# Optimization experiments

Hardware: AMD Instinct MI355X
Metric: run time of the kernel (lower is better)

## Reference

```python
import jax, jax.numpy as jnp
import numpy as np

B, H, W = 16, 512, 512  # mask resolution; feature maps are 2H x 2W


def setup_inputs() -> dict:
    key = jax.random.key(0)
    k0, k1, k2, k3, k4 = jax.random.split(key, 5)
    mask = jax.random.uniform(k0, (B, 2, H, W), dtype=jnp.float32)
    xl_out = jax.random.normal(k1, (B, 3, 2 * H, 2 * W), dtype=jnp.float32)
    yl_out = jax.random.normal(k2, (B, 3, 2 * H, 2 * W), dtype=jnp.float32)
    conv_w = jax.random.normal(k3, (3, 3), dtype=jnp.float32) * 0.1  # 1x1 conv [out_c, in_c]
    conv_b = jax.random.normal(k4, (3,), dtype=jnp.float32) * 0.1
    return {"mask": mask, "xl_out": xl_out, "yl_out": yl_out,
            "conv_w": conv_w, "conv_b": conv_b}


def reference(mask, xl_out, yl_out, conv_w, conv_b):
    b, _, h, w = mask.shape
    up = jax.image.resize(mask, (b, 2, 2 * h, 2 * w), method="bilinear")  # [B,2,2H,2W]
    x_mask = up[:, 0:1]  # [B,1,2H,2W]
    y_mask = up[:, 1:2]
    fused = x_mask * xl_out + y_mask * yl_out  # [B,3,2H,2W]
    # 1x1 conv == channel mixing matmul, then ReLU.
    out = jnp.einsum("oi,bihw->bohw", conv_w, fused) + conv_b[None, :, None, None]
    out = jax.nn.relu(out)
    return (out, x_mask, y_mask)
```

## Files before the change

kernel.cpp:

```cpp
#include <hip/hip_runtime.h>

#define BATCH 16
#define HIN   512
#define WIN   512
#define HOUT  1024
#define WOUT  1024

#define OUT_ELEMS   ((size_t)BATCH * 3 * HOUT * WOUT)
#define MASK_ELEMS  ((size_t)BATCH * HOUT * WOUT)

typedef float f4 __attribute__((ext_vector_type(4)));

static __device__ __forceinline__ f4 relu4(f4 v) {
    v.x = fmaxf(v.x, 0.0f); v.y = fmaxf(v.y, 0.0f);
    v.z = fmaxf(v.z, 0.0f); v.w = fmaxf(v.w, 0.0f);
    return v;
}

__global__ __launch_bounds__(256) void fused_upsample_conv_kernel(
    const float* __restrict__ mask,
    const float* __restrict__ xl,
    const float* __restrict__ yl,
    const float* __restrict__ cw,
    const float* __restrict__ cb,
    float* __restrict__ out)
{
    const int tx   = threadIdx.x;
    const int half = tx >> 7;
    const int lane = tx & 127;
    const int r    = blockIdx.x;
    const int b    = blockIdx.y;
    const int oh   = 2 * r + half;

    int rA, rB; float wyA, wyB;
    if (half) { rA = r;                   rB = (r + 1 < HIN) ? r + 1 : HIN - 1; wyA = 0.75f; wyB = 0.25f; }
    else      { rA = (r > 0) ? r - 1 : 0; rB = r;                               wyA = 0.25f; wyB = 0.75f; }

    const int c0 = lane * 4;
    const int cL = (c0 > 0) ? c0 - 1 : 0;
    const int cR = (c0 + 4 < WIN) ? c0 + 4 : WIN - 1;

    const size_t mplane = (size_t)HIN * WIN;
    const float* pA0 = mask + ((size_t)b * 2 + 0) * mplane + (size_t)rA * WIN;
    const float* pB0 = mask + ((size_t)b * 2 + 0) * mplane + (size_t)rB * WIN;
    const float* pA1 = mask + ((size_t)b * 2 + 1) * mplane + (size_t)rA * WIN;
    const float* pB1 = mask + ((size_t)b * 2 + 1) * mplane + (size_t)rB * WIN;

    const f4    qA0 = *(const f4*)(pA0 + c0);
    const f4    qB0 = *(const f4*)(pB0 + c0);
    const float vL0 = wyA * pA0[cL] + wyB * pB0[cL];
    const float vR0 = wyA * pA0[cR] + wyB * pB0[cR];
    const f4    v0  = wyA * qA0 + wyB * qB0;

    const f4    qA1 = *(const f4*)(pA1 + c0);
    const f4    qB1 = *(const f4*)(pB1 + c0);
    const float vL1 = wyA * pA1[cL] + wyB * pB1[cL];
    const float vR1 = wyA * pA1[cR] + wyB * pB1[cR];
    const f4    v1  = wyA * qA1 + wyB * qB1;

    f4 xm0, xm1, ym0, ym1;
    xm0.x = 0.25f*vL0  + 0.75f*v0.x;  xm0.y = 0.75f*v0.x + 0.25f*v0.y;
    xm0.z = 0.25f*v0.x + 0.75f*v0.y;  xm0.w = 0.75f*v0.y + 0.25f*v0.z;
    xm1.x = 0.25f*v0.y + 0.75f*v0.z;  xm1.y = 0.75f*v0.z + 0.25f*v0.w;
    xm1.z = 0.25f*v0.z + 0.75f*v0.w;  xm1.w = 0.75f*v0.w + 0.25f*vR0;

    ym0.x = 0.25f*vL1  + 0.75f*v1.x;  ym0.y = 0.75f*v1.x + 0.25f*v1.y;
    ym0.z = 0.25f*v1.x + 0.75f*v1.y;  ym0.w = 0.75f*v1.y + 0.25f*v1.z;
    ym1.x = 0.25f*v1.y + 0.75f*v1.z;  ym1.y = 0.75f*v1.z + 0.25f*v1.w;
    ym1.z = 0.25f*v1.z + 0.75f*v1.w;  ym1.w = 0.75f*v1.w + 0.25f*vR1;

    const float w00 = cw[0], w01 = cw[1], w02 = cw[2];
    const float w10 = cw[3], w11 = cw[4], w12 = cw[5];
    const float w20 = cw[6], w21 = cw[7], w22 = cw[8];
    const float b0 = cb[0], b1 = cb[1], b2 = cb[2];

    const size_t oplane = (size_t)HOUT * WOUT;
    const size_t rowoff = (size_t)oh * WOUT + (size_t)lane * 8;

    const float* xb = xl + ((size_t)b * 3) * oplane + rowoff;
    const float* yb = yl + ((size_t)b * 3) * oplane + rowoff;

    const f4 x00 = __builtin_nontemporal_load((const f4*)(xb + 0 * oplane));
    const f4 x01 = __builtin_nontemporal_load((const f4*)(xb + 0 * oplane) + 1);
    const f4 x10 = __builtin_nontemporal_load((const f4*)(xb + 1 * oplane));
    const f4 x11 = __builtin_nontemporal_load((const f4*)(xb + 1 * oplane) + 1);
    const f4 x20 = __builtin_nontemporal_load((const f4*)(xb + 2 * oplane));
    const f4 x21 = __builtin_nontemporal_load((const f4*)(xb + 2 * oplane) + 1);
    const f4 y00 = __builtin_nontemporal_load((const f4*)(yb + 0 * oplane));
    const f4 y01 = __builtin_nontemporal_load((const f4*)(yb + 0 * oplane) + 1);
    const f4 y10 = __builtin_nontemporal_load((const f4*)(yb + 1 * oplane));
    const f4 y11 = __builtin_nontemporal_load((const f4*)(yb + 1 * oplane) + 1);
    const f4 y20 = __builtin_nontemporal_load((const f4*)(yb + 2 * oplane));
    const f4 y21 = __builtin_nontemporal_load((const f4*)(yb + 2 * oplane) + 1);

    const f4 f00 = xm0 * x00 + ym0 * y00;
    const f4 f01 = xm1 * x01 + ym1 * y01;
    const f4 f10 = xm0 * x10 + ym0 * y10;
    const f4 f11 = xm1 * x11 + ym1 * y11;
    const f4 f20 = xm0 * x20 + ym0 * y20;
    const f4 f21 = xm1 * x21 + ym1 * y21;

    const f4 o00 = relu4(w00*f00 + w01*f10 + w02*f20 + b0);
    const f4 o01 = relu4(w00*f01 + w01*f11 + w02*f21 + b0);
    const f4 o10 = relu4(w10*f00 + w11*f10 + w12*f20 + b1);
    const f4 o11 = relu4(w10*f01 + w11*f11 + w12*f21 + b1);
    const f4 o20 = relu4(w20*f00 + w21*f10 + w22*f20 + b2);
    const f4 o21 = relu4(w20*f01 + w21*f11 + w22*f21 + b2);

    float* ob = out + ((size_t)b * 3) * oplane + rowoff;
    __builtin_nontemporal_store(o00, (f4*)(ob + 0 * oplane));
    __builtin_nontemporal_store(o01, (f4*)(ob + 0 * oplane) + 1);
    __builtin_nontemporal_store(o10, (f4*)(ob + 1 * oplane));
    __builtin_nontemporal_store(o11, (f4*)(ob + 1 * oplane) + 1);
    __builtin_nontemporal_store(o20, (f4*)(ob + 2 * oplane));
    __builtin_nontemporal_store(o21, (f4*)(ob + 2 * oplane) + 1);

    float* xmp = out + OUT_ELEMS + (size_t)b * oplane + rowoff;
    float* ymp = out + OUT_ELEMS + MASK_ELEMS + (size_t)b * oplane + rowoff;
    __builtin_nontemporal_store(xm0, (f4*)xmp);
    __builtin_nontemporal_store(xm1, (f4*)xmp + 1);
    __builtin_nontemporal_store(ym0, (f4*)ymp);
    __builtin_nontemporal_store(ym1, (f4*)ymp + 1);
}

extern "C" void kernel_launch(void* const* d_in, const int* in_sizes, int n_in,
                              void* d_out, int out_size, void* d_ws, size_t ws_size,
                              hipStream_t stream) {
    const float* mask = (const float*)d_in[0];
    const float* xl   = (const float*)d_in[1];
    const float* yl   = (const float*)d_in[2];
    const float* cw   = (const float*)d_in[3];
    const float* cb   = (const float*)d_in[4];
    float* out = (float*)d_out;

    dim3 grid(HOUT / 2, BATCH);
    dim3 block(256);
    fused_upsample_conv_kernel<<<grid, block, 0, stream>>>(mask, xl, yl, cw, cb, out);
}
```

Measured before the change: 595.6 us.

## Specialize waves per plane/mask channel with LDS staging of masks and fused features

Restructures the block into 8 waves: six waves each stream one channel row of xl/yl with fully contiguous per-wave loads, while two waves compute the upsampled x/y masks for both output rows into LDS. After barriers the fused features are staged in LDS so each wave computes one output channel of the 1x1 conv and writes it. This aims for longer contiguous memory streams and less redundant mask work per thread, at the cost of two block barriers, about 40KB LDS per block, and the two mask waves doing different work from the others.

Result: faster. 580.3 us (-2.6%).

```diff
diff --git a/kernel.cpp b/kernel.cpp
--- a/kernel.cpp
+++ b/kernel.cpp
@@ -17,7 +17,7 @@
     return v;
 }
 
-__global__ __launch_bounds__(256) void fused_upsample_conv_kernel(
+__global__ __launch_bounds__(512, 4) void fused_upsample_conv_kernel(
     const float* __restrict__ mask,
     const float* __restrict__ xl,
     const float* __restrict__ yl,
@@ -25,102 +25,129 @@
     const float* __restrict__ cb,
     float* __restrict__ out)
 {
-    const int tx   = threadIdx.x;
-    const int half = tx >> 7;
-    const int lane = tx & 127;
-    const int r    = blockIdx.x;
-    const int b    = blockIdx.y;
-    const int oh   = 2 * r + half;
+    __shared__ float xm_l[2][WOUT];
+    __shared__ float ym_l[2][WOUT];
+    __shared__ float Fs[3][2][WOUT];
 
-    int rA, rB; float wyA, wyB;
-    if (half) { rA = r;                   rB = (r + 1 < HIN) ? r + 1 : HIN - 1; wyA = 0.75f; wyB = 0.25f; }
-    else      { rA = (r > 0) ? r - 1 : 0; rB = r;                               wyA = 0.25f; wyB = 0.75f; }
-
-    const int c0 = lane * 4;
-    const int cL = (c0 > 0) ? c0 - 1 : 0;
-    const int cR = (c0 + 4 < WIN) ? c0 + 4 : WIN - 1;
-
-    const size_t mplane = (size_t)HIN * WIN;
-    const float* pA0 = mask + ((size_t)b * 2 + 0) * mplane + (size_t)rA * WIN;
-    const float* pB0 = mask + ((size_t)b * 2 + 0) * mplane + (size_t)rB * WIN;
-    const float* pA1 = mask + ((size_t)b * 2 + 1) * mplane + (size_t)rA * WIN;
-    const float* pB1 = mask + ((size_t)b * 2 + 1) * mplane + (size_t)rB * WIN;
-
-    const f4    qA0 = *(const f4*)(pA0 + c0);
-    const f4    qB0 = *(const f4*)(pB0 + c0);
-    const float vL0 = wyA * pA0[cL] + wyB * pB0[cL];
-    const float vR0 = wyA * pA0[cR] + wyB * pB0[cR];
-    const f4    v0  = wyA * qA0 + wyB * qB0;
-
-    const f4    qA1 = *(const f4*)(pA1 + c0);
-    const f4    qB1 = *(const f4*)(pB1 + c0);
-    const float vL1 = wyA * pA1[cL] + wyB * pB1[cL];
-    const float vR1 = wyA * pA1[cR] + wyB * pB1[cR];
-    const f4    v1  = wyA * qA1 + wyB * qB1;
-
-    f4 xm0, xm1, ym0, ym1;
-    xm0.x = 0.25f*vL0  + 0.75f*v0.x;  xm0.y = 0.75f*v0.x + 0.25f*v0.y;
-    xm0.z = 0.25f*v0.x + 0.75f*v0.y;  xm0.w = 0.75f*v0.y + 0.25f*v0.z;
-    xm1.x = 0.25f*v0.y + 0.75f*v0.z;  xm1.y = 0.75f*v0.z + 0.25f*v0.w;
-    xm1.z = 0.25f*v0.z + 0.75f*v0.w;  xm1.w = 0.75f*v0.w + 0.25f*vR0;
-
-    ym0.x = 0.25f*vL1  + 0.75f*v1.x;  ym0.y = 0.75f*v1.x + 0.25f*v1.y;
-    ym0.z = 0.25f*v1.x + 0.75f*v1.y;  ym0.w = 0.75f*v1.y + 0.25f*v1.z;
-    ym1.x = 0.25f*v1.y + 0.75f*v1.z;  ym1.y = 0.75f*v1.z + 0.25f*v1.w;
-    ym1.z = 0.25f*v1.z + 0.75f*v1.w;  ym1.w = 0.75f*v1.w + 0.25f*vR1;
-
-    const float w00 = cw[0], w01 = cw[1], w02 = cw[2];
-    const float w10 = cw[3], w11 = cw[4], w12 = cw[5];
-    const float w20 = cw[6], w21 = cw[7], w22 = cw[8];
-    const float b0 = cb[0], b1 = cb[1], b2 = cb[2];
+    const int tx = threadIdx.x;
+    const int w  = tx >> 6;
+    const int l  = tx & 63;
+    const int r  = blockIdx.x;
+    const int b  = blockIdx.y;
 
     const size_t oplane = (size_t)HOUT * WOUT;
-    const size_t rowoff = (size_t)oh * WOUT + (size_t)lane * 8;
+    const size_t mplane = (size_t)HIN * WIN;
 
-    const float* xb = xl + ((size_t)b * 3) * oplane + rowoff;
-    const float* yb = yl + ((size_t)b * 3) * oplane + rowoff;
+    const int p  = w % 3;
+    const int hr = (w < 6) ? (w / 3) : 0;
+    const int oh = 2 * r + hr;
 
-    const f4 x00 = __builtin_nontemporal_load((const f4*)(xb + 0 * oplane));
-    const f4 x01 = __builtin_nontemporal_load((const f4*)(xb + 0 * oplane) + 1);
-    const f4 x10 = __builtin_nontemporal_load((const f4*)(xb + 1 * oplane));
-    const f4 x11 = __builtin_nontemporal_load((const f4*)(xb + 1 * oplane) + 1);
-    const f4 x20 = __builtin_nontemporal_load((const f4*)(xb + 2 * oplane));
-    const f4 x21 = __builtin_nontemporal_load((const f4*)(xb + 2 * oplane) + 1);
-    const f4 y00 = __builtin_nontemporal_load((const f4*)(yb + 0 * oplane));
-    const f4 y01 = __builtin_nontemporal_load((const f4*)(yb + 0 * oplane) + 1);
-    const f4 y10 = __builtin_nontemporal_load((const f4*)(yb + 1 * oplane));
-    const f4 y11 = __builtin_nontemporal_load((const f4*)(yb + 1 * oplane) + 1);
-    const f4 y20 = __builtin_nontemporal_load((const f4*)(yb + 2 * oplane));
-    const f4 y21 = __builtin_nontemporal_load((const f4*)(yb + 2 * oplane) + 1);
+    f4 xv0, xv1, xv2, xv3, yv0, yv1, yv2, yv3;
 
-    const f4 f00 = xm0 * x00 + ym0 * y00;
-    const f4 f01 = xm1 * x01 + ym1 * y01;
-    const f4 f10 = xm0 * x10 + ym0 * y10;
-    const f4 f11 = xm1 * x11 + ym1 * y11;
-    const f4 f20 = xm0 * x20 + ym0 * y20;
-    const f4 f21 = xm1 * x21 + ym1 * y21;
+    if (w < 6) {
+        const float* xp = xl + ((size_t)b * 3 + p) * oplane + (size_t)oh * WOUT;
+        const float* yp = yl + ((size_t)b * 3 + p) * oplane + (size_t)oh * WOUT;
+        xv0 = __builtin_nontemporal_load((const f4*)(xp +   0) + l);
+        xv1 = __builtin_nontemporal_load((const f4*)(xp + 256) + l);
+        xv2 = __builtin_nontemporal_load((const f4*)(xp + 512) + l);
+        xv3 = __builtin_nontemporal_load((const f4*)(xp + 768) + l);
+        yv0 = __builtin_nontemporal_load((const f4*)(yp +   0) + l);
+        yv1 = __builtin_nontemporal_load((const f4*)(yp + 256) + l);
+        yv2 = __builtin_nontemporal_load((const f4*)(yp + 512) + l);
+        yv3 = __builtin_nontemporal_load((const f4*)(yp + 768) + l);
+    } else {
+        const int ch = w - 6;
+        const float* mp = mask + ((size_t)b * 2 + ch) * mplane;
+        const int rm = (r > 0) ? r - 1 : 0;
+        const int rp = (r + 1 < HIN) ? r + 1 : HIN - 1;
+        const float* rowm = mp + (size_t)rm * WIN;
+        const float* row0 = mp + (size_t)r  * WIN;
+        const float* rowp = mp + (size_t)rp * WIN;
 
-    const f4 o00 = relu4(w00*f00 + w01*f10 + w02*f20 + b0);
-    const f4 o01 = relu4(w00*f01 + w01*f11 + w02*f21 + b0);
-    const f4 o10 = relu4(w10*f00 + w11*f10 + w12*f20 + b1);
-    const f4 o11 = relu4(w10*f01 + w11*f11 + w12*f21 + b1);
-    const f4 o20 = relu4(w20*f00 + w21*f10 + w22*f20 + b2);
-    const f4 o21 = relu4(w20*f01 + w21*f11 + w22*f21 + b2);
+        const int c0 = l * 8;
+        const int cL = (c0 > 0) ? c0 - 1 : 0;
+        const int cR = (c0 + 8 < WIN) ? c0 + 8 : WIN - 1;
 
-    float* ob = out + ((size_t)b * 3) * oplane + rowoff;
-    __builtin_nontemporal_store(o00, (f4*)(ob + 0 * oplane));
-    __builtin_nontemporal_store(o01, (f4*)(ob + 0 * oplane) + 1);
-    __builtin_nontemporal_store(o10, (f4*)(ob + 1 * oplane));
-    __builtin_nontemporal_store(o11, (f4*)(ob + 1 * oplane) + 1);
-    __builtin_nontemporal_store(o20, (f4*)(ob + 2 * oplane));
-    __builtin_nontemporal_store(o21, (f4*)(ob + 2 * oplane) + 1);
+        const f4 ma0 = *(const f4*)(rowm + c0), ma1 = *(const f4*)(rowm + c0 + 4);
+        const f4 za0 = *(const f4*)(row0 + c0), za1 = *(const f4*)(row0 + c0 + 4);
+        const f4 pa0 = *(const f4*)(rowp + c0), pa1 = *(const f4*)(rowp + c0 + 4);
+        const float mL = rowm[cL], mR = rowm[cR];
+        const float zL = row0[cL], zR = row0[cR];
+        const float pL = rowp[cL], pR = rowp[cR];
 
-    float* xmp = out + OUT_ELEMS + (size_t)b * oplane + rowoff;
-    float* ymp = out + OUT_ELEMS + MASK_ELEMS + (size_t)b * oplane + rowoff;
-    __builtin_nontemporal_store(xm0, (f4*)xmp);
-    __builtin_nontemporal_store(xm1, (f4*)xmp + 1);
-    __builtin_nontemporal_store(ym0, (f4*)ymp);
-    __builtin_nontemporal_store(ym1, (f4*)ymp + 1);
+        float* base = ch ? &ym_l[0][0] : &xm_l[0][0];
+
+        #pragma unroll
+        for (int rr = 0; rr < 2; ++rr) {
+            f4 va, vb; float vL, vR;
+            if (rr == 0) {
+                va = 0.25f * ma0 + 0.75f * za0;  vb = 0.25f * ma1 + 0.75f * za1;
+                vL = 0.25f * mL  + 0.75f * zL;   vR = 0.25f * mR  + 0.75f * zR;
+            } else {
+                va = 0.75f * za0 + 0.25f * pa0;  vb = 0.75f * za1 + 0.25f * pa1;
+                vL = 0.75f * zL  + 0.25f * pL;   vR = 0.75f * zR  + 0.25f * pR;
+            }
+            f4 o0, o1, o2, o3;
+            o0.x = 0.25f*vL   + 0.75f*va.x;  o0.y = 0.75f*va.x + 0.25f*va.y;
+            o0.z = 0.25f*va.x + 0.75f*va.y;  o0.w = 0.75f*va.y + 0.25f*va.z;
+            o1.x = 0.25f*va.y + 0.75f*va.z;  o1.y = 0.75f*va.z + 0.25f*va.w;
+            o1.z = 0.25f*va.z + 0.75f*va.w;  o1.w = 0.75f*va.w + 0.25f*vb.x;
+            o2.x = 0.25f*va.w + 0.75f*vb.x;  o2.y = 0.75f*vb.x + 0.25f*vb.y;
+            o2.z = 0.25f*vb.x + 0.75f*vb.y;  o2.w = 0.75f*vb.y + 0.25f*vb.z;
+            o3.x = 0.25f*vb.y + 0.75f*vb.z;  o3.y = 0.75f*vb.z + 0.25f*vb.w;
+            o3.z = 0.25f*vb.z + 0.75f*vb.w;  o3.w = 0.75f*vb.w + 0.25f*vR;
+            float* d = base + rr * WOUT + l * 16;
+            *(f4*)(d +  0) = o0;  *(f4*)(d +  4) = o1;
+            *(f4*)(d +  8) = o2;  *(f4*)(d + 12) = o3;
+        }
+    }
+
+    __syncthreads();
+
+    if (w < 6) {
+        const float* mx = &xm_l[hr][0];
+        const float* my = &ym_l[hr][0];
+        float* fd = &Fs[p][hr][0];
+        const int c = l * 4;
+        *(f4*)(fd + c +   0) = (*(const f4*)(mx + c +   0)) * xv0 + (*(const f4*)(my + c +   0)) * yv0;
+        *(f4*)(fd + c + 256) = (*(const f4*)(mx + c + 256)) * xv1 + (*(const f4*)(my + c + 256)) * yv1;
+        *(f4*)(fd + c + 512) = (*(const f4*)(mx + c + 512)) * xv2 + (*(const f4*)(my + c + 512)) * yv2;
+        *(f4*)(fd + c + 768) = (*(const f4*)(mx + c + 768)) * xv3 + (*(const f4*)(my + c + 768)) * yv3;
+    }
+
+    __syncthreads();
+
+    if (w < 6) {
+        const float w0 = cw[p * 3 + 0], w1 = cw[p * 3 + 1], w2 = cw[p * 3 + 2];
+        const float bo = cb[p];
+        float* op = out + ((size_t)b * 3 + p) * oplane + (size_t)oh * WOUT;
+        const float* F0 = &Fs[0][hr][0];
+        const float* F1 = &Fs[1][hr][0];
+        const float* F2 = &Fs[2][hr][0];
+        #pragma unroll
+        for (int k = 0; k < 4; ++k) {
+            const int c = k * 256 + l * 4;
+            const f4 a0 = *(const f4*)(F0 + c);
+            const f4 a1 = *(const f4*)(F1 + c);
+            const f4 a2 = *(const f4*)(F2 + c);
+            const f4 o  = relu4(w0 * a0 + w1 * a1 + w2 * a2 + bo);
+            __builtin_nontemporal_store(o, (f4*)(op + c));
+        }
+    } else {
+        const int ch = w - 6;
+        const float* src = ch ? &ym_l[0][0] : &xm_l[0][0];
+        float* op = out + OUT_ELEMS + (size_t)ch * MASK_ELEMS
+                  + (size_t)b * oplane + (size_t)(2 * r) * WOUT;
+        #pragma unroll
+        for (int rr = 0; rr < 2; ++rr) {
+            #pragma unroll
+            for (int k = 0; k < 4; ++k) {
+                const int c = k * 256 + l * 4;
+                const f4 v = *(const f4*)(src + rr * WOUT + c);
+                __builtin_nontemporal_store(v, (f4*)(op + rr * WOUT + c));
+            }
+        }
+    }
 }
 
 extern "C" void kernel_launch(void* const* d_in, const int* in_sizes, int n_in,
@@ -133,7 +160,7 @@
     const float* cb   = (const float*)d_in[4];
     float* out = (float*)d_out;
 
-    dim3 grid(HOUT / 2, BATCH);
-    dim3 block(256);
+    dim3 grid(HIN, BATCH);
+    dim3 block(512);
     fused_upsample_conv_kernel<<<grid, block, 0, stream>>>(mask, xl, yl, cw, cb, out);
 }
```
